# Kernel optimization log

Hardware: AMD Instinct MI355X
Metric: run time of the kernel (lower is better)

The kernel has to match this reference:

```python
import jax, jax.numpy as jnp
import numpy as np

UNITS = 512

def _lstm_layer(x, W, U, b):
    # x: [B,T,D], W: [D,4H], U: [H,4H], b: [4H]. Keras gate order: i,f,g(c),o.
    B = x.shape[0]
    H = U.shape[0]
    xW = jnp.einsum('btd,dk->btk', x, W) + b  # precompute input projection
    def step(carry, xw_t):
        h, c = carry
        z = xw_t + h @ U
        i, f, g, o = jnp.split(z, 4, axis=-1)
        i = jax.nn.sigmoid(i)
        f = jax.nn.sigmoid(f)
        g = jnp.tanh(g)
        o = jax.nn.sigmoid(o)
        c = f * c + i * g
        h = o * jnp.tanh(c)
        return (h, c), h
    h0 = jnp.zeros((B, H), x.dtype)
    c0 = jnp.zeros((B, H), x.dtype)
    (h, c), hs = jax.lax.scan(step, (h0, c0), jnp.swapaxes(xW, 0, 1))
    return jnp.swapaxes(hs, 0, 1), h, c  # seq [B,T,H], final h, final c


def setup_inputs() -> dict:
    key = jax.random.key(0)
    ks = jax.random.split(key, 10)
    B, T, D, H = 64, 512, 256, UNITS
    s = lambda fan_in: 1.0 / np.sqrt(fan_in)
    inp = {
        'inputs': jax.random.normal(ks[0], (B, T, D), dtype=jnp.float32),
        'W0': jax.random.normal(ks[1], (D, 4 * H), dtype=jnp.float32) * s(D),
        'U0': jax.random.normal(ks[2], (H, 4 * H), dtype=jnp.float32) * s(H),
        'b0': jnp.zeros((4 * H,), jnp.float32),
        'W1': jax.random.normal(ks[3], (H, 4 * H), dtype=jnp.float32) * s(H),
        'U1': jax.random.normal(ks[4], (H, 4 * H), dtype=jnp.float32) * s(H),
        'b1': jnp.zeros((4 * H,), jnp.float32),
        'W2': jax.random.normal(ks[5], (H, 4 * H), dtype=jnp.float32) * s(H),
        'U2': jax.random.normal(ks[6], (H, 4 * H), dtype=jnp.float32) * s(H),
        'b2': jnp.zeros((4 * H,), jnp.float32),
    }
    return inp


def reference(inputs, W0, U0, b0, W1, U1, b1, W2, U2, b2):
    # Layer 0 and 1 return full sequences; layer 2 returns only final state.
    # Dropout is identity at inference (training=None in original call).
    x, h0, c0 = _lstm_layer(inputs, W0, U0, b0)
    x, h1, c1 = _lstm_layer(x, W1, U1, b1)
    _, h2, c2 = _lstm_layer(x, W2, U2, b2)
    out = h2  # last layer: return_sequences=False -> final hidden state
    return (out, h0, c0, h1, c1, h2, c2)
```

## Files before the change

kernel.cpp:

```cpp
#include <hip/hip_runtime.h>
#include <hip/hip_bf16.h>


#define BB 64
#define TT 512
#define DD 256
#define HH 512
#define GG 2048
#define SS (BB * HH)
#define NBLK 256
#define NTHR 512
#define RL 8
#define KPAD 1032
#define ZLD 516
#define POLL_CAP 20000
#define SPIN_CAP (1 << 20)

using short8 = __attribute__((ext_vector_type(8))) short;
using f32x4  = __attribute__((ext_vector_type(4))) float;
using f4     = f32x4;
using u32x2  = __attribute__((ext_vector_type(2))) unsigned;

__device__ unsigned long long g_word = 0;
__device__ unsigned g_cnt[8] = {};

__device__ __forceinline__ short f2bf(float f) {
  unsigned u = __builtin_bit_cast(unsigned, f);
  u = (u + 0x7fffu + ((u >> 16) & 1u)) >> 16;
  return (short)u;
}
__device__ __forceinline__ float sigm(float x)  { return 1.f / (1.f + __expf(-x)); }
__device__ __forceinline__ float tanh_(float x) { return 2.f / (1.f + __expf(-2.f * x)) - 1.f; }

__device__ __forceinline__ short8 pack8(const f4& lo, const f4& hi) {
  return (short8){f2bf(lo[0]), f2bf(lo[1]), f2bf(lo[2]), f2bf(lo[3]),
                  f2bf(hi[0]), f2bf(hi[1]), f2bf(hi[2]), f2bf(hi[3])};
}

__device__ __forceinline__ void stH(void* p, unsigned v) {
  asm volatile("global_store_dword %0, %1, off sc0 sc1" :: "v"(p), "v"(v) : "memory");
}
__device__ __forceinline__ void stH2(void* p, u32x2 v) {
  asm volatile("global_store_dwordx2 %0, %1, off sc0 sc1" :: "v"(p), "v"(v) : "memory");
}
__device__ __forceinline__ void stS(void* p, unsigned v) {
  asm volatile("global_store_dword %0, %1, off sc0" :: "v"(p), "v"(v) : "memory");
}
__device__ __forceinline__ int ld_icc(const int* p) {
  int v;
  asm volatile("global_load_dword %0, %1, off sc0 sc1\n\ts_waitcnt vmcnt(0)"
               : "=v"(v) : "v"(p) : "memory");
  return v;
}
__device__ __forceinline__ unsigned atom_rd(unsigned* p) {
  unsigned old, zero = 0;
  asm volatile("global_atomic_add %0, %1, %2, off sc0\n\ts_waitcnt vmcnt(0)"
               : "=v"(old) : "v"(p), "v"(zero) : "memory");
  return old;
}
__device__ __forceinline__ void atom_add1(unsigned* p) {
  unsigned one = 1;
  asm volatile("global_atomic_add %0, %1, off" :: "v"(p), "v"(one) : "memory");
}
#define INV() asm volatile("buffer_inv sc0\n\ts_waitcnt vmcnt(0)" ::: "memory")

#define ISSUE4_A0(A, P)                                                        \
  asm volatile("global_load_dwordx4 %0, %4, off\n\t"                           \
               "global_load_dwordx4 %1, %4, off offset:512\n\t"                \
               "global_load_dwordx4 %2, %4, off offset:1024\n\t"               \
               "global_load_dwordx4 %3, %4, off offset:1536"                   \
               : "=&v"(A[0]), "=&v"(A[1]), "=&v"(A[2]), "=&v"(A[3]) : "v"(P))
#define ISSUE4_AH(A, P)                                                        \
  asm volatile("global_load_dwordx4 %0, %4, off sc0 sc1\n\t"                   \
               "global_load_dwordx4 %1, %4, off offset:512 sc0 sc1\n\t"        \
               "global_load_dwordx4 %2, %4, off offset:1024 sc0 sc1\n\t"       \
               "global_load_dwordx4 %3, %4, off offset:1536 sc0 sc1"           \
               : "=&v"(A[0]), "=&v"(A[1]), "=&v"(A[2]), "=&v"(A[3]) : "v"(P))

#define ISSUE_X(X, O0, O1, P)                                                    \
  asm volatile("global_load_dwordx4 %0, %8, off offset:" #O0 "\n\t"              \
               "global_load_dwordx4 %1, %8, off offset:" #O1 "\n\t"              \
               "global_load_dwordx4 %2, %9, off offset:" #O0 "\n\t"              \
               "global_load_dwordx4 %3, %9, off offset:" #O1 "\n\t"              \
               "global_load_dwordx4 %4, %10, off offset:" #O0 "\n\t"             \
               "global_load_dwordx4 %5, %10, off offset:" #O1 "\n\t"             \
               "global_load_dwordx4 %6, %11, off offset:" #O0 "\n\t"             \
               "global_load_dwordx4 %7, %11, off offset:" #O1                    \
               : "=&v"(X[0]), "=&v"(X[1]), "=&v"(X[2]), "=&v"(X[3]),             \
                 "=&v"(X[4]), "=&v"(X[5]), "=&v"(X[6]), "=&v"(X[7])              \
               : "v"(P[0]), "v"(P[1]), "v"(P[2]), "v"(P[3]))

#define WAIT4(N, A)                                                              \
  asm volatile("s_waitcnt vmcnt(" #N ")"                                         \
               : "+v"(A[0]), "+v"(A[1]), "+v"(A[2]), "+v"(A[3]))
#define WAIT8(N, X)                                                              \
  asm volatile("s_waitcnt vmcnt(" #N ")"                                         \
               : "+v"(X[0]), "+v"(X[1]), "+v"(X[2]), "+v"(X[3]),                 \
                 "+v"(X[4]), "+v"(X[5]), "+v"(X[6]), "+v"(X[7]))

#define MFMA_S(AV, S_)                                                           \
  do {                                                                           \
    _Pragma("unroll")                                                            \
    for (int mt_ = 0; mt_ < 4; ++mt_) {                                          \
      _Pragma("unroll")                                                          \
      for (int g_ = 0; g_ < 4; ++g_)                                             \
        acc[mt_][g_] = __builtin_amdgcn_mfma_f32_16x16x32_bf16(                  \
            (AV)[mt_], bF[g_][S_], acc[mt_][g_], 0, 0, 0);                       \
    }                                                                            \
  } while (0)

#define SELF_SEQ(ISS, PBASE)                                                     \
  do {                                                                           \
    short8 u0[4], u1[4];                                                         \
    ISS(u0, (PBASE));                                                            \
    ISS(u1, (PBASE) + 4096);                                                     \
    WAIT4(4, u0); MFMA_S(u0, 0); ISS(u0, (PBASE) + 8192);                        \
    WAIT4(4, u1); MFMA_S(u1, 1); ISS(u1, (PBASE) + 12288);                       \
    WAIT4(4, u0); MFMA_S(u0, 2);                                                 \
    WAIT4(0, u1); MFMA_S(u1, 3);                                                 \
  } while (0)

__device__ __forceinline__ void grid_barrier(unsigned target) {
  asm volatile("s_waitcnt vmcnt(0)" ::: "memory");
  __syncthreads();
  if (threadIdx.x == 0) {
    unsigned long long old = __hip_atomic_fetch_add(&g_word, 1ull, __ATOMIC_RELAXED,
                                                    __HIP_MEMORY_SCOPE_AGENT);
    if ((unsigned)(old & 0xffffffffull) == NBLK - 1) {
      __hip_atomic_fetch_add(&g_word, (1ull << 32) - (unsigned long long)NBLK,
                             __ATOMIC_RELAXED, __HIP_MEMORY_SCOPE_AGENT);
    } else {
      while ((int)((unsigned)(__hip_atomic_load(&g_word, __ATOMIC_RELAXED,
                                                __HIP_MEMORY_SCOPE_AGENT) >> 32) - target) < 0)
        __builtin_amdgcn_s_sleep(2);
    }
  }
  __syncthreads();
}

extern "C" __global__ __launch_bounds__(NTHR, 2) void lstm_persistent(
    const float* __restrict__ x,
    const float* __restrict__ W0, const float* __restrict__ U0, const float* __restrict__ b0,
    const float* __restrict__ W1, const float* __restrict__ U1, const float* __restrict__ b1,
    const float* __restrict__ W2, const float* __restrict__ U2, const float* __restrict__ b2,
    float* __restrict__ out,
    int* __restrict__ flags,
    unsigned short* __restrict__ hbufL,
    unsigned short* __restrict__ hbufR,
    int big, int rrm)
{
  __shared__ __align__(16) char smem[64 * ZLD * 4];
  unsigned short (*Wl)[KPAD] = (unsigned short (*)[KPAD])smem;
  float (*Zpt)[ZLD] = (float (*)[ZLD])smem;
  __shared__ float biasl[64];
  __shared__ unsigned hpk[NTHR];
  __shared__ int s_l, s_sl, s_bgo, s_go;
  __shared__ unsigned s_gen0;

  const int tid = threadIdx.x;

  if (tid == 0) {
    s_gen0 = (unsigned)(__hip_atomic_load(&g_word, __ATOMIC_RELAXED,
                                          __HIP_MEMORY_SCOPE_AGENT) >> 32);
    unsigned xid;
    asm volatile("s_getreg_b32 %0, hwreg(HW_REG_XCC_ID)" : "=s"(xid));
    const int xcd = (int)(xid & 7u);
    unsigned r = __hip_atomic_fetch_add(&g_cnt[xcd], 1u, __ATOMIC_RELAXED,
                                        __HIP_MEMORY_SCOPE_AGENT);
    s_l = (xcd < 3) ? xcd : -1;
    s_sl = (int)(r & 31u);
    s_bgo = -1;
    s_go = -1;
  }
  __syncthreads();
  const int l = s_l;
  const int slice = s_sl;
  if (l < 0) { grid_barrier(s_gen0 + 1); return; }

  const float* Wsrc = (l == 0) ? W0 : (l == 1) ? W1 : W2;
  const float* Usrc = (l == 0) ? U0 : (l == 1) ? U1 : U2;
  const float* bsrc = (l == 0) ? b0 : (l == 1) ? b1 : b2;
  const int Kx = (l == 0) ? DD : HH;
  const int j0g = slice * 16;

  #define SLAB_L(LL, T_) (hbufL + (size_t)((LL) * RL + ((T_) & (RL - 1))) * SS)
  #define SLAB_R(BB_, T_) (hbufR + (size_t)((BB_) * (rrm + 1) + ((T_) & rrm)) * SS)

  int* fl_glob  = (int*)((char*)flags + 1024 + (size_t)l * 256);
  int* fl_gprev = (l > 0) ? (int*)((char*)flags + 1024 + (size_t)(l - 1) * 256) : fl_glob;
  int* fl_gnext = (l < 2) ? (int*)((char*)flags + 1024 + (size_t)(l + 1) * 256) : fl_glob;
  unsigned* cntp = (unsigned*)((char*)flags + 2048 + (size_t)l * 128);

  unsigned cbase = 0;
  if (tid == 256) cbase = atom_rd(cntp);

  for (int q = 0; q < 8; ++q) {
    const int gcol = (q >> 1) * HH + j0g + (q & 1) * 8;
    for (int k = tid; k < Kx; k += NTHR) {
      const float* s = Wsrc + (size_t)k * GG + gcol;
      #pragma unroll
      for (int c = 0; c < 8; ++c) Wl[q * 8 + c][k] = (unsigned short)f2bf(s[c]);
    }
    for (int k = tid; k < HH; k += NTHR) {
      const float* s = Usrc + (size_t)k * GG + gcol;
      #pragma unroll
      for (int c = 0; c < 8; ++c) Wl[q * 8 + c][Kx + k] = (unsigned short)f2bf(s[c]);
    }
  }
  if (tid < 64) biasl[tid] = bsrc[(tid >> 4) * HH + j0g + (tid & 15)];

  { unsigned* z = (unsigned*)(SLAB_L(l, -1) + slice * 1024); stS(z + tid, 0u); }
  if (slice == 0 && tid < 32) stH(fl_glob + tid, 0u);
  __syncthreads();

  const int lane = tid & 63;
  const int wv   = tid >> 6;
  const int quad = lane >> 4;
  const int m    = lane & 15;
  const int col  = m;
  const bool selfw = (wv >= 4);
  int kbase;
  if (l == 0) kbase = selfw ? 256 + 128 * (wv - 4) : 64 * wv;
  else        kbase = selfw ? 512 + 128 * (wv - 4) : 128 * wv;

  short8 bF[4][4];
  #pragma unroll
  for (int g = 0; g < 4; ++g)
    #pragma unroll
    for (int s = 0; s < 4; ++s)
      bF[g][s] = *(const short8*)&Wl[g * 16 + col][kbase + 32 * s + quad * 8];

  grid_barrier(s_gen0 + 1);

  const size_t laneoff  = (size_t)(quad >> 1) * 2048 + (size_t)(quad & 1) * 16 + (size_t)m * 32;
  const size_t selfoff  = (size_t)(128 * (wv - 4)) * 128 + laneoff;
  const size_t belowoff = (size_t)(128 * wv) * 128 + laneoff;

  const int* pb = fl_gprev + (lane & 31);
  const int* pa = fl_gnext + (lane & 31);

  float cR[2] = {0.f, 0.f};
  int fbs = -1;
  int fas = -1;

  for (int t = 0; t < TT; ++t) {
    f32x4 acc[4][4];
    #pragma unroll
    for (int a_ = 0; a_ < 4; ++a_)
      #pragma unroll
      for (int g_ = 0; g_ < 4; ++g_) acc[a_][g_] = (f32x4){0.f, 0.f, 0.f, 0.f};

    if (selfw) {
      if (tid == 256) {
        const unsigned tgt = cbase + 32u * (unsigned)t;
        for (int it = 0; it < POLL_CAP; ++it)
          if ((int)(atom_rd(cntp) - tgt) >= 0) break;
        ((volatile int*)&s_go)[0] = t;
      }
      { int sp = 0;
        while (((volatile int*)&s_go)[0] < t && sp < SPIN_CAP) ++sp; }
      INV();
      const char* pp0 = (const char*)SLAB_L(l, t - 1) + selfoff;
      SELF_SEQ(ISSUE4_A0, pp0);
    } else if (l > 0) {
      if (wv == 0) {
        const bool needb = __any(fbs < t + 1);
        const bool needa = (!big && l == 1) ? __any(fas < t - rrm) : false;
        if (needb || needa) {
          for (int it = 0; it < POLL_CAP; ++it) {
            fbs = ld_icc(pb);
            if (!big && l == 1) fas = ld_icc(pa);
            bool ok = (fbs >= t + 1);
            if (!big && l == 1) ok = ok && (fas >= t - rrm);
            if (__all(ok)) break;
            __builtin_amdgcn_s_sleep(1);
          }
        }
        ((volatile int*)&s_bgo)[0] = t;
      } else {
        int sp = 0;
        while (((volatile int*)&s_bgo)[0] < t && sp < SPIN_CAP) ++sp;
      }
      const char* pp0 = (const char*)SLAB_R(l - 1, t) + belowoff;
      if (big) { SELF_SEQ(ISSUE4_A0, pp0); }
      else     { SELF_SEQ(ISSUE4_AH, pp0); }
    } else {
      if (!big && wv == 0) {
        if (__any(fas < t - rrm)) {
          for (int it = 0; it < POLL_CAP; ++it) {
            fas = ld_icc(pa);
            if (__all(fas >= t - rrm)) break;
            __builtin_amdgcn_s_sleep(1);
          }
        }
      }
      const float* pX[4];
      #pragma unroll
      for (int mt = 0; mt < 4; ++mt)
        pX[mt] = x + ((size_t)(16 * mt + m) * TT + t) * DD + wv * 64 + quad * 8;
      f4 xv0[8], xv1[8];
      ISSUE_X(xv0, 0, 16, pX);
      ISSUE_X(xv1, 128, 144, pX);
      WAIT8(8, xv0);
      { short8 a2[4] = {pack8(xv0[0], xv0[1]), pack8(xv0[2], xv0[3]),
                        pack8(xv0[4], xv0[5]), pack8(xv0[6], xv0[7])};
        MFMA_S(a2, 0); }
      WAIT8(0, xv1);
      { short8 a2[4] = {pack8(xv1[0], xv1[1]), pack8(xv1[2], xv1[3]),
                        pack8(xv1[4], xv1[5]), pack8(xv1[6], xv1[7])};
        MFMA_S(a2, 1); }
    }

    #pragma unroll
    for (int mt = 0; mt < 4; ++mt)
      #pragma unroll
      for (int g = 0; g < 4; ++g)
        *(f32x4*)&Zpt[g * 16 + col][wv * 64 + 16 * mt + 4 * quad] = acc[mt][g];

    __syncthreads();

    if (tid == 0) stH(fl_glob + slice, (unsigned)t);

    {
      const int b_ = tid >> 3;
      const int hp = tid & 7;
      float zz[2][4];
      #pragma unroll
      for (int g = 0; g < 4; ++g) {
        zz[0][g] = biasl[g * 16 + 2 * hp];
        zz[1][g] = biasl[g * 16 + 2 * hp + 1];
      }
      #pragma unroll
      for (int w = 0; w < 8; ++w)
        #pragma unroll
        for (int g = 0; g < 4; ++g) {
          zz[0][g] += Zpt[g * 16 + 2 * hp    ][w * 64 + b_];
          zz[1][g] += Zpt[g * 16 + 2 * hp + 1][w * 64 + b_];
        }
      float hh2[2], cc2[2];
      #pragma unroll
      for (int e = 0; e < 2; ++e) {
        const float gi = sigm(zz[e][0]), gf = sigm(zz[e][1]);
        const float gz = tanh_(zz[e][2]), go = sigm(zz[e][3]);
        const float cc = gf * cR[e] + gi * gz;
        cR[e] = cc; cc2[e] = cc;
        hh2[e] = go * tanh_(cc);
      }
      const unsigned pk = (unsigned)(unsigned short)f2bf(hh2[0]) |
                          ((unsigned)(unsigned short)f2bf(hh2[1]) << 16);
      hpk[tid] = pk;
      unsigned* dL = (unsigned*)(SLAB_L(l, t) + slice * 1024);
      stS(dL + tid, pk);
      if (t == TT - 1) {
        const int oi = b_ * HH + j0g + 2 * hp;
        if (l == 0) {
          out[SS + oi] = hh2[0];      out[SS + oi + 1] = hh2[1];
          out[2 * SS + oi] = cc2[0];  out[2 * SS + oi + 1] = cc2[1];
        } else if (l == 1) {
          out[3 * SS + oi] = hh2[0];  out[3 * SS + oi + 1] = hh2[1];
          out[4 * SS + oi] = cc2[0];  out[4 * SS + oi + 1] = cc2[1];
        } else {
          out[oi] = hh2[0];           out[oi + 1] = hh2[1];
          out[5 * SS + oi] = hh2[0];  out[5 * SS + oi + 1] = hh2[1];
          out[6 * SS + oi] = cc2[0];  out[6 * SS + oi + 1] = cc2[1];
        }
      }
    }

    asm volatile("s_waitcnt vmcnt(0)" ::: "memory");
    __syncthreads();

    if (tid == 0) atom_add1(cntp);
    if (!selfw && l < 2) {
      u32x2 hv = *(const u32x2*)&hpk[2 * tid];
      unsigned* dR = (unsigned*)(SLAB_R(l, t) + slice * 1024) + 2 * tid;
      stH2(dR, hv);
    }
  }

  asm volatile("s_waitcnt vmcnt(0)" ::: "memory");
  __syncthreads();
  if (tid == 0) stH(fl_glob + slice, (unsigned)TT);

  #undef SLAB_L
  #undef SLAB_R
}

extern "C" void kernel_launch(void* const* d_in, const int* in_sizes, int n_in,
                              void* d_out, int out_size, void* d_ws, size_t ws_size,
                              hipStream_t stream) {
  const float* x  = (const float*)d_in[0];
  const float* W0 = (const float*)d_in[1];
  const float* U0 = (const float*)d_in[2];
  const float* b0 = (const float*)d_in[3];
  const float* W1 = (const float*)d_in[4];
  const float* U1 = (const float*)d_in[5];
  const float* b1 = (const float*)d_in[6];
  const float* W2 = (const float*)d_in[7];
  const float* U2 = (const float*)d_in[8];
  const float* b2 = (const float*)d_in[9];
  float* out = (float*)d_out;
  int* flags = (int*)d_ws;
  unsigned short* hbufL = (unsigned short*)((char*)d_ws + 4096);
  unsigned short* hbufR = hbufL + (size_t)3 * RL * SS;

  const size_t need_big = 4096 + (size_t)3 * RL * SS * 2 + (size_t)2 * TT * SS * 2;
  int big = (ws_size >= need_big) ? 1 : 0;
  int rrm = big ? (TT - 1) : 15;

  void* args[] = {(void*)&x,
                  (void*)&W0, (void*)&U0, (void*)&b0,
                  (void*)&W1, (void*)&U1, (void*)&b1,
                  (void*)&W2, (void*)&U2, (void*)&b2,
                  (void*)&out, (void*)&flags, (void*)&hbufL, (void*)&hbufR,
                  (void*)&big, (void*)&rrm};
  hipLaunchCooperativeKernel((void*)lstm_persistent, dim3(NBLK), dim3(NTHR),
                             args, 0, stream);
}
```

Before: 2.789 ms.

## Prefetch cross-layer progress flag asynchronously and wait for initial slack before the loop

Wave 0 of layers above the first now issues a non-blocking flag load for the layer below at the end of each step and folds its completion into the last vmcnt wait of the MFMA sequence, so the poll latency overlaps compute. Before the loop it waits until the lower layer is a few steps ahead, which reduces stalls later. The progress flag store moves after the h-slab writes and the counter increment, giving a stricter publish ordering. The risk is reading a stale flag, which falls back to the existing polling loop, and the store move may delay consumers slightly.

Measured after the change: 2.823 ms. Within noise of the previous version (+1.2%).

```diff
diff --git a/kernel.cpp b/kernel.cpp
--- a/kernel.cpp
+++ b/kernel.cpp
@@ -15,6 +15,7 @@
 #define ZLD 516
 #define POLL_CAP 20000
 #define SPIN_CAP (1 << 20)
+#define SLACK0 4
 
 using short8 = __attribute__((ext_vector_type(8))) short;
 using f32x4  = __attribute__((ext_vector_type(4))) float;
@@ -118,6 +119,20 @@
     WAIT4(4, u1); MFMA_S(u1, 1); ISS(u1, (PBASE) + 12288);                       \
     WAIT4(4, u0); MFMA_S(u0, 2);                                                 \
     WAIT4(0, u1); MFMA_S(u1, 3);                                                 \
+  } while (0)
+
+#define SELF_SEQ_F(ISS, PBASE, FR)                                               \
+  do {                                                                           \
+    short8 u0[4], u1[4];                                                         \
+    ISS(u0, (PBASE));                                                            \
+    ISS(u1, (PBASE) + 4096);                                                     \
+    WAIT4(4, u0); MFMA_S(u0, 0); ISS(u0, (PBASE) + 8192);                        \
+    WAIT4(4, u1); MFMA_S(u1, 1); ISS(u1, (PBASE) + 12288);                       \
+    WAIT4(4, u0); MFMA_S(u0, 2);                                                 \
+    asm volatile("s_waitcnt vmcnt(0)"                                            \
+                 : "+v"(u1[0]), "+v"(u1[1]), "+v"(u1[2]), "+v"(u1[3]),           \
+                   "+v"(FR));                                                    \
+    MFMA_S(u1, 3);                                                               \
   } while (0)
 
 __device__ __forceinline__ void grid_barrier(unsigned target) {
@@ -183,6 +198,9 @@
   const int Kx = (l == 0) ? DD : HH;
   const int j0g = slice * 16;
 
+  const int lane = tid & 63;
+  const int wv   = tid >> 6;
+
   #define SLAB_L(LL, T_) (hbufL + (size_t)((LL) * RL + ((T_) & (RL - 1))) * SS)
   #define SLAB_R(BB_, T_) (hbufR + (size_t)((BB_) * (rrm + 1) + ((T_) & rrm)) * SS)
 
@@ -213,8 +231,6 @@
   if (slice == 0 && tid < 32) stH(fl_glob + tid, 0u);
   __syncthreads();
 
-  const int lane = tid & 63;
-  const int wv   = tid >> 6;
   const int quad = lane >> 4;
   const int m    = lane & 15;
   const int col  = m;
@@ -242,6 +258,16 @@
   float cR[2] = {0.f, 0.f};
   int fbs = -1;
   int fas = -1;
+  int F   = -1;
+
+  if (l > 0 && wv == 0) {
+    for (int it = 0; it < POLL_CAP; ++it) {
+      fbs = ld_icc(pb);
+      if (__all(fbs >= SLACK0)) break;
+      __builtin_amdgcn_s_sleep(2);
+    }
+    F = fbs;
+  }
 
   for (int t = 0; t < TT; ++t) {
     f32x4 acc[4][4];
@@ -277,13 +303,17 @@
           }
         }
         ((volatile int*)&s_bgo)[0] = t;
+        const char* pp0 = (const char*)SLAB_R(l - 1, t) + belowoff;
+        if (big) { SELF_SEQ_F(ISSUE4_A0, pp0, F); }
+        else     { SELF_SEQ_F(ISSUE4_AH, pp0, F); }
+        fbs = F;
       } else {
         int sp = 0;
         while (((volatile int*)&s_bgo)[0] < t && sp < SPIN_CAP) ++sp;
-      }
-      const char* pp0 = (const char*)SLAB_R(l - 1, t) + belowoff;
-      if (big) { SELF_SEQ(ISSUE4_A0, pp0); }
-      else     { SELF_SEQ(ISSUE4_AH, pp0); }
+        const char* pp0 = (const char*)SLAB_R(l - 1, t) + belowoff;
+        if (big) { SELF_SEQ(ISSUE4_A0, pp0); }
+        else     { SELF_SEQ(ISSUE4_AH, pp0); }
+      }
     } else {
       if (!big && wv == 0) {
         if (__any(fas < t - rrm)) {
@@ -318,8 +348,6 @@
         *(f32x4*)&Zpt[g * 16 + col][wv * 64 + 16 * mt + 4 * quad] = acc[mt][g];
 
     __syncthreads();
-
-    if (tid == 0) stH(fl_glob + slice, (unsigned)t);
 
     {
       const int b_ = tid >> 3;
@@ -370,7 +398,13 @@
     asm volatile("s_waitcnt vmcnt(0)" ::: "memory");
     __syncthreads();
 
-    if (tid == 0) atom_add1(cntp);
+    if (tid == 0) {
+      atom_add1(cntp);
+      stH(fl_glob + slice, (unsigned)t);
+    }
+    if (l > 0 && wv == 0)
+      asm volatile("global_load_dword %0, %1, off sc0 sc1"
+                   : "=v"(F) : "v"(pb) : "memory");
     if (!selfw && l < 2) {
       u32x2 hv = *(const u32x2*)&hpk[2 * tid];
       unsigned* dR = (unsigned*)(SLAB_R(l, t) + slice * 1024) + 2 * tid;
```
